# Kernel tuning notes

Hardware: AMD Instinct MI355X
Metric: run time of the kernel (lower is better)

## Reference

```python
import jax, jax.numpy as jnp
import numpy as np

DIM = 17  # LUT grid resolution per axis


def quad_interp(lut, x):
    """Quadrilinear (4D) LUT interpolation.
    lut: [C_out, D, D, D, D]; x: [B, 4, H, W] with values expected in [0, 1].
    Returns [B, C_out, H, W].
    """
    D = lut.shape[1]
    xs = jnp.clip(x, 0.0, 1.0) * (D - 1)          # [B,4,H,W]
    i0 = jnp.clip(jnp.floor(xs).astype(jnp.int32), 0, D - 2)
    f = xs - i0.astype(xs.dtype)                   # fractional part in [0,1]
    idx = [i0[:, k] for k in range(4)]             # each [B,H,W]
    frc = [f[:, k] for k in range(4)]
    out = None
    for corner in range(16):  # fixed 16-corner loop, not a data-dim loop
        ids, w = [], None
        for k in range(4):
            b = (corner >> k) & 1
            ids.append(idx[k] + b)
            wk = frc[k] if b else (1.0 - frc[k])
            w = wk if w is None else w * wk
        v = lut[:, ids[0], ids[1], ids[2], ids[3]]  # gather -> [C,B,H,W]
        term = v * w[None]
        out = term if out is None else out + term
    return jnp.transpose(out, (1, 0, 2, 3))        # [B,C,H,W]


def setup_inputs() -> dict:
    key = jax.random.key(0)
    ks = jax.random.split(key, 8)
    B, H, W = 8, 512, 512
    vi_image = jax.random.uniform(ks[0], (B, 3, H, W), dtype=jnp.float32)
    ir_image = jax.random.uniform(ks[1], (B, 1, H, W), dtype=jnp.float32)
    # Learned LUT tables (identity-style grids would live in [0,1]; use uniform)
    g = (DIM, DIM, DIM, DIM)
    lut8 = jax.random.uniform(ks[2], (4,) + g, dtype=jnp.float32)
    lut00 = jax.random.uniform(ks[3], (4,) + g, dtype=jnp.float32)
    lut01 = jax.random.uniform(ks[4], (4,) + g, dtype=jnp.float32)
    lut02 = jax.random.uniform(ks[5], (4,) + g, dtype=jnp.float32)
    lut03 = jax.random.uniform(ks[6], (4,) + g, dtype=jnp.float32)
    lutpgf = jax.random.uniform(ks[7], (3,) + g, dtype=jnp.float32)
    return {"vi_image": vi_image, "ir_image": ir_image, "lut8": lut8,
            "lut00": lut00, "lut01": lut01, "lut02": lut02,
            "lut03": lut03, "lutpgf": lutpgf}


def reference(vi_image, ir_image, lut8, lut00, lut01, lut02, lut03, lutpgf):
    x = jnp.concatenate([vi_image, ir_image], axis=1)   # [B,4,H,W]
    x = jnp.clip(quad_interp(lut8, x), 0.0, 1.0)        # hardtanh(0,1)
    x = jnp.clip(quad_interp(lut00, x), 0.0, 1.0)
    x = jnp.clip(quad_interp(lut01, x), 0.0, 1.0)
    x = jnp.clip(quad_interp(lut02, x), 0.0, 1.0)
    x = jnp.clip(quad_interp(lut03, x), 0.0, 1.0)
    return quad_interp(lutpgf, x)                       # [B,3,H,W]
```

## Files before the change

kernel.cpp:

```cpp
#include <hip/hip_runtime.h>

#pragma clang fp contract(off)

#define D4    83521
#define HW    262144
#define NPIX  2097152
#define QREC  73984
#define RECN  69632
#define CBLK  64

struct SrcPtrs { const float* p[6]; };

__global__ __launch_bounds__(256) void pack_oct_all(SrcPtrs sp,
                                                    float4* __restrict__ dst) {
    const int PER = RECN * 8;
    int j = blockIdx.x * 256 + threadIdx.x;
    int s = j / PER;
    int r = j - s * PER;
    int g = r & 7;
    int e = r >> 3;
    int i3 = e & 15;
    int i2 = (e >> 4) & 15;
    int i1 = (e >> 8) & 15;
    int i0 = e >> 12;
    int o = i0 * 4913 + i1 * 289 + i2 * 17 + i3
          + ((g >> 2) & 1) * 289 + ((g >> 1) & 1) * 17 + (g & 1);
    const float* __restrict__ src = sp.p[s];
    float4 v;
    v.x = src[o];
    v.y = src[D4 + o];
    v.z = src[2 * D4 + o];
    v.w = (s != 5) ? src[3 * D4 + o] : 0.f;
    dst[j] = v;
}

__global__ __launch_bounds__(CBLK) void fused_coop(const float* __restrict__ vi,
                                                   const float* __restrict__ ir,
                                                   const float4* __restrict__ luts,
                                                   float* __restrict__ out) {
#pragma clang fp contract(off)
    __shared__ float4 exch[CBLK * 17];

    int tid = threadIdx.x;
    int p = blockIdx.x * CBLK + tid;
    int b  = p >> 18;
    int hw = p & (HW - 1);
    int vbase = (b * 3) << 18;

    float x0 = vi[vbase + hw];
    float x1 = vi[vbase + HW + hw];
    float x2 = vi[vbase + 2 * HW + hw];
    float x3 = ir[p];

    int sub  = tid >> 4;
    int kidx = tid & 15;
    int b0   = (kidx >> 2) & 1;
    int slot = ((kidx >> 3) & 1) * 4 + (kidx & 1) * 2 + ((kidx >> 1) & 1);

    for (int s = 0; s < 6; ++s) {
        const float4* __restrict__ lutS =
            luts + (size_t)s * (RECN * 8) + b0 * (4096 * 8) + slot;

        x0 = fminf(fmaxf(x0, 0.f), 1.f);
        x1 = fminf(fmaxf(x1, 0.f), 1.f);
        x2 = fminf(fmaxf(x2, 0.f), 1.f);
        x3 = fminf(fmaxf(x3, 0.f), 1.f);
        float xs0 = x0 * 16.f;
        float xs1 = x1 * 16.f;
        float xs2 = x2 * 16.f;
        float xs3 = x3 * 16.f;
        int i0 = (int)xs0; i0 = i0 > 15 ? 15 : i0;
        int i1 = (int)xs1; i1 = i1 > 15 ? 15 : i1;
        int i2 = (int)xs2; i2 = i2 > 15 ? 15 : i2;
        int i3 = (int)xs3; i3 = i3 > 15 ? 15 : i3;
        float f0 = xs0 - (float)i0;
        float f1 = xs1 - (float)i1;
        float f2 = xs2 - (float)i2;
        float f3 = xs3 - (float)i3;
        float g0 = 1.f - f0;
        float g1 = 1.f - f1;
        float g2 = 1.f - f2;
        float g3 = 1.f - f3;
        float w01[4] = { g0 * g1, f0 * g1, g0 * f1, f0 * f1 };

        int r00 = ((i0 * 16 + i1) * 16 + i2) * 16 + i3;

        int r0s[16];
#pragma unroll
        for (int t = 0; t < 16; ++t)
            r0s[t] = __shfl(r00, 4 * t + sub, 64);

        float4 v[16];
#pragma unroll
        for (int t = 0; t < 16; ++t)
            v[t] = lutS[(size_t)r0s[t] * 8];
        __builtin_amdgcn_sched_barrier(0);

#pragma unroll
        for (int t = 0; t < 16; ++t)
            exch[(4 * t + sub) * 17 + kidx] = v[t];
        __builtin_amdgcn_sched_barrier(0);

        const float4* myb = &exch[tid * 17];
        float a0 = 0.f, a1 = 0.f, a2 = 0.f, a3 = 0.f;
#pragma unroll
        for (int hi = 0; hi < 2; ++hi) {
            float w3 = hi ? f3 : g3;
#pragma unroll
            for (int c = 0; c < 8; ++c) {
                int k = ((c & 3) << 2) + ((c >> 2) + 2 * hi);
                float4 vv = myb[k];
                float w012 = w01[c & 3] * ((c >> 2) ? f2 : g2);
                float w    = w012 * w3;
                if (hi == 0 && c == 0) {
                    a0 = vv.x * w; a1 = vv.y * w; a2 = vv.z * w; a3 = vv.w * w;
                } else {
                    a0 = a0 + vv.x * w; a1 = a1 + vv.y * w;
                    a2 = a2 + vv.z * w; a3 = a3 + vv.w * w;
                }
            }
        }
        __builtin_amdgcn_sched_barrier(0);
        x0 = a0; x1 = a1; x2 = a2; x3 = a3;
    }

    out[vbase + hw]          = x0;
    out[vbase + HW + hw]     = x1;
    out[vbase + 2 * HW + hw] = x2;
}

__global__ __launch_bounds__(256) void pack_quad(const float* __restrict__ src,
                                                 int n_ch,
                                                 float4* __restrict__ dst) {
    int e = blockIdx.x * 256 + threadIdx.x;
    if (e >= QREC) return;
    int i3 = e & 15;
    int i2 = (e >> 4) & 15;
    int t  = e >> 8;
    int i0 = t / 17;
    int i1 = t - i0 * 17;
    int base = i0 * 4913 + i1 * 289 + i2 * 17 + i3;
    float4* rec = dst + (size_t)e * 4;
#pragma unroll
    for (int g = 0; g < 4; ++g) {
        int o = base + (g & 1) * 17 + (g >> 1);
        float4 v;
        v.x = src[o];
        v.y = src[D4 + o];
        v.z = src[2 * D4 + o];
        v.w = (n_ch == 4) ? src[3 * D4 + o] : 0.f;
        rec[g] = v;
    }
}

__global__ __launch_bounds__(CBLK) void fused_coop_q(const float* __restrict__ vi,
                                                     const float* __restrict__ ir,
                                                     const float4* __restrict__ luts,
                                                     float* __restrict__ out) {
#pragma clang fp contract(off)
    __shared__ float4 exch[CBLK * 17];

    int tid = threadIdx.x;
    int p = blockIdx.x * CBLK + tid;
    int b  = p >> 18;
    int hw = p & (HW - 1);
    int vbase = (b * 3) << 18;

    float x0 = vi[vbase + hw];
    float x1 = vi[vbase + HW + hw];
    float x2 = vi[vbase + 2 * HW + hw];
    float x3 = ir[p];

    int rec     = (tid >> 2) & 3;
    int slot    = tid & 3;
    int rec_off = ((rec & 1) ? 4352 : 0) + ((rec & 2) ? 256 : 0);
    int sub     = tid >> 4;
    int kidx    = tid & 15;

    for (int s = 0; s < 6; ++s) {
        const float4* __restrict__ lutS =
            luts + (size_t)s * QREC * 4 + (size_t)rec_off * 4 + slot;

        x0 = fminf(fmaxf(x0, 0.f), 1.f);
        x1 = fminf(fmaxf(x1, 0.f), 1.f);
        x2 = fminf(fmaxf(x2, 0.f), 1.f);
        x3 = fminf(fmaxf(x3, 0.f), 1.f);
        float xs0 = x0 * 16.f;
        float xs1 = x1 * 16.f;
        float xs2 = x2 * 16.f;
        float xs3 = x3 * 16.f;
        int i0 = (int)xs0; i0 = i0 > 15 ? 15 : i0;
        int i1 = (int)xs1; i1 = i1 > 15 ? 15 : i1;
        int i2 = (int)xs2; i2 = i2 > 15 ? 15 : i2;
        int i3 = (int)xs3; i3 = i3 > 15 ? 15 : i3;
        float f0 = xs0 - (float)i0;
        float f1 = xs1 - (float)i1;
        float f2 = xs2 - (float)i2;
        float f3 = xs3 - (float)i3;
        float g0 = 1.f - f0;
        float g1 = 1.f - f1;
        float g2 = 1.f - f2;
        float g3 = 1.f - f3;
        float w01[4] = { g0 * g1, f0 * g1, g0 * f1, f0 * f1 };

        int r00 = ((i0 * 17 + i1) * 16 + i2) * 16 + i3;

        int r0s[16];
#pragma unroll
        for (int t = 0; t < 16; ++t)
            r0s[t] = __shfl(r00, 4 * t + sub, 64);

        float4 v[16];
#pragma unroll
        for (int t = 0; t < 16; ++t)
            v[t] = lutS[(size_t)r0s[t] * 4];
        __builtin_amdgcn_sched_barrier(0);

#pragma unroll
        for (int t = 0; t < 16; ++t)
            exch[(4 * t + sub) * 17 + kidx] = v[t];
        __builtin_amdgcn_sched_barrier(0);

        const float4* myb = &exch[tid * 17];
        float a0 = 0.f, a1 = 0.f, a2 = 0.f, a3 = 0.f;
#pragma unroll
        for (int hi = 0; hi < 2; ++hi) {
            float w3 = hi ? f3 : g3;
#pragma unroll
            for (int c = 0; c < 8; ++c) {
                int k = ((c & 3) << 2) + ((c >> 2) + 2 * hi);
                float4 vv = myb[k];
                float w012 = w01[c & 3] * ((c >> 2) ? f2 : g2);
                float w    = w012 * w3;
                if (hi == 0 && c == 0) {
                    a0 = vv.x * w; a1 = vv.y * w; a2 = vv.z * w; a3 = vv.w * w;
                } else {
                    a0 = a0 + vv.x * w; a1 = a1 + vv.y * w;
                    a2 = a2 + vv.z * w; a3 = a3 + vv.w * w;
                }
            }
        }
        __builtin_amdgcn_sched_barrier(0);
        x0 = a0; x1 = a1; x2 = a2; x3 = a3;
    }

    out[vbase + hw]          = x0;
    out[vbase + HW + hw]     = x1;
    out[vbase + 2 * HW + hw] = x2;
}

__global__ __launch_bounds__(256) void fused_fallback(const float* __restrict__ vi,
                                                      const float* __restrict__ ir,
                                                      const float* __restrict__ l8,
                                                      const float* __restrict__ l00,
                                                      const float* __restrict__ l01,
                                                      const float* __restrict__ l02,
                                                      const float* __restrict__ l03,
                                                      const float* __restrict__ lpgf,
                                                      float* __restrict__ out) {
#pragma clang fp contract(off)
    int p = blockIdx.x * 256 + threadIdx.x;
    if (p >= NPIX) return;
    int b  = p >> 18;
    int hw = p & (HW - 1);
    int vbase = (b * 3) << 18;

    const float* ptrs[6] = { l8, l00, l01, l02, l03, lpgf };

    float x0 = vi[vbase + hw];
    float x1 = vi[vbase + HW + hw];
    float x2 = vi[vbase + 2 * HW + hw];
    float x3 = ir[p];

    for (int s = 0; s < 6; ++s) {
        const float* __restrict__ L = ptrs[s];
        int n_ch = (s == 5) ? 3 : 4;
        x0 = fminf(fmaxf(x0, 0.f), 1.f);
        x1 = fminf(fmaxf(x1, 0.f), 1.f);
        x2 = fminf(fmaxf(x2, 0.f), 1.f);
        x3 = fminf(fmaxf(x3, 0.f), 1.f);
        float xs0 = x0 * 16.f;
        float xs1 = x1 * 16.f;
        float xs2 = x2 * 16.f;
        float xs3 = x3 * 16.f;
        int i0 = (int)xs0; i0 = i0 > 15 ? 15 : i0;
        int i1 = (int)xs1; i1 = i1 > 15 ? 15 : i1;
        int i2 = (int)xs2; i2 = i2 > 15 ? 15 : i2;
        int i3 = (int)xs3; i3 = i3 > 15 ? 15 : i3;
        float f0 = xs0 - (float)i0;
        float f1 = xs1 - (float)i1;
        float f2 = xs2 - (float)i2;
        float f3 = xs3 - (float)i3;
        float g0 = 1.f - f0;
        float g1 = 1.f - f1;
        float g2 = 1.f - f2;
        float g3 = 1.f - f3;
        float w01[4] = { g0 * g1, f0 * g1, g0 * f1, f0 * f1 };
        int off = i0 * 4913 + i1 * 289 + i2 * 17 + i3;
        float a0 = 0.f, a1 = 0.f, a2 = 0.f, a3 = 0.f;
        for (int cr = 0; cr < 16; ++cr) {
            int hi = cr >> 3, c = cr & 7;
            int idx = off + (c & 1) * 4913 + ((c >> 1) & 1) * 289 + (c >> 2) * 17 + hi;
            float w012 = w01[c & 3] * ((c >> 2) ? f2 : g2);
            float w    = w012 * (hi ? f3 : g3);
            float v0 = L[idx];
            float v1 = L[D4 + idx];
            float v2 = L[2 * D4 + idx];
            float v3 = (n_ch == 4) ? L[3 * D4 + idx] : 0.f;
            if (cr == 0) {
                a0 = v0 * w; a1 = v1 * w; a2 = v2 * w; a3 = v3 * w;
            } else {
                a0 = a0 + v0 * w; a1 = a1 + v1 * w;
                a2 = a2 + v2 * w; a3 = a3 + v3 * w;
            }
        }
        x0 = a0; x1 = a1; x2 = a2; x3 = a3;
    }

    out[vbase + hw]          = x0;
    out[vbase + HW + hw]     = x1;
    out[vbase + 2 * HW + hw] = x2;
}

extern "C" void kernel_launch(void* const* d_in, const int* in_sizes, int n_in,
                              void* d_out, int out_size, void* d_ws, size_t ws_size,
                              hipStream_t stream) {
    const float* vi = (const float*)d_in[0];
    const float* ir = (const float*)d_in[1];
    const float* raw[6] = {
        (const float*)d_in[2], (const float*)d_in[3],
        (const float*)d_in[4], (const float*)d_in[5],
        (const float*)d_in[6], (const float*)d_in[7]
    };
    float* out = (float*)d_out;

    const size_t OSZ      = (size_t)RECN * 128;
    const size_t NEED_OCT = 6 * OSZ;
    const size_t QSZ      = (size_t)QREC * 64;
    const size_t NEED_Q   = 6 * QSZ;

    if (ws_size >= NEED_OCT) {
        SrcPtrs sp;
        for (int s = 0; s < 6; ++s) sp.p[s] = raw[s];
        int pack_blocks = 6 * RECN * 8 / 256;
        pack_oct_all<<<pack_blocks, 256, 0, stream>>>(sp, (float4*)d_ws);
        fused_coop<<<NPIX / CBLK, CBLK, 0, stream>>>(vi, ir, (const float4*)d_ws, out);
    } else if (ws_size >= NEED_Q) {
        char* ws = (char*)d_ws;
        int pack_blocks = (QREC + 255) / 256;
        for (int s = 0; s < 6; ++s) {
            pack_quad<<<pack_blocks, 256, 0, stream>>>(raw[s], (s == 5) ? 3 : 4,
                                                       (float4*)(ws + s * QSZ));
        }
        fused_coop_q<<<NPIX / CBLK, CBLK, 0, stream>>>(vi, ir, (const float4*)ws, out);
    } else {
        fused_fallback<<<NPIX / 256, 256, 0, stream>>>(vi, ir, raw[0], raw[1], raw[2],
                                                       raw[3], raw[4], raw[5], out);
    }
}
```

Baseline: 278.8 us.

## Halve LDS exchange buffer by two-phase exchange and add occupancy hint

Splits the cooperative LDS exchange into two halves that reuse a 32-pixel buffer, so the shared-memory footprint per block is halved. Each half of the wavefront accumulates its interpolation in turn. The change also adds a min-blocks launch bound and replaces a per-thread integer division in the LUT pack kernel with a per-block one. More blocks should fit per CU, but half the lanes sit idle during each accumulation phase, which serializes the compute work.

```diff
diff --git a/kernel.cpp b/kernel.cpp
--- a/kernel.cpp
+++ b/kernel.cpp
@@ -14,8 +14,9 @@
 __global__ __launch_bounds__(256) void pack_oct_all(SrcPtrs sp,
                                                     float4* __restrict__ dst) {
     const int PER = RECN * 8;
-    int j = blockIdx.x * 256 + threadIdx.x;
-    int s = j / PER;
+    int blk = blockIdx.x;
+    int s = blk / 2176;
+    int j = blk * 256 + threadIdx.x;
     int r = j - s * PER;
     int g = r & 7;
     int e = r >> 3;
@@ -34,12 +35,12 @@
     dst[j] = v;
 }
 
-__global__ __launch_bounds__(CBLK) void fused_coop(const float* __restrict__ vi,
-                                                   const float* __restrict__ ir,
-                                                   const float4* __restrict__ luts,
-                                                   float* __restrict__ out) {
+__global__ __launch_bounds__(CBLK, 4) void fused_coop(const float* __restrict__ vi,
+                                                      const float* __restrict__ ir,
+                                                      const float4* __restrict__ luts,
+                                                      float* __restrict__ out) {
 #pragma clang fp contract(off)
-    __shared__ float4 exch[CBLK * 17];
+    __shared__ float4 exch[32 * 17];
 
     int tid = threadIdx.x;
     int p = blockIdx.x * CBLK + tid;
@@ -96,31 +97,62 @@
             v[t] = lutS[(size_t)r0s[t] * 8];
         __builtin_amdgcn_sched_barrier(0);
 
-#pragma unroll
-        for (int t = 0; t < 16; ++t)
+        float a0 = 0.f, a1 = 0.f, a2 = 0.f, a3 = 0.f;
+
+#pragma unroll
+        for (int t = 0; t < 8; ++t)
             exch[(4 * t + sub) * 17 + kidx] = v[t];
         __builtin_amdgcn_sched_barrier(0);
 
-        const float4* myb = &exch[tid * 17];
-        float a0 = 0.f, a1 = 0.f, a2 = 0.f, a3 = 0.f;
-#pragma unroll
-        for (int hi = 0; hi < 2; ++hi) {
-            float w3 = hi ? f3 : g3;
-#pragma unroll
-            for (int c = 0; c < 8; ++c) {
-                int k = ((c & 3) << 2) + ((c >> 2) + 2 * hi);
-                float4 vv = myb[k];
-                float w012 = w01[c & 3] * ((c >> 2) ? f2 : g2);
-                float w    = w012 * w3;
-                if (hi == 0 && c == 0) {
-                    a0 = vv.x * w; a1 = vv.y * w; a2 = vv.z * w; a3 = vv.w * w;
-                } else {
-                    a0 = a0 + vv.x * w; a1 = a1 + vv.y * w;
-                    a2 = a2 + vv.z * w; a3 = a3 + vv.w * w;
+        if (tid < 32) {
+            const float4* myb = &exch[tid * 17];
+#pragma unroll
+            for (int hi = 0; hi < 2; ++hi) {
+                float w3 = hi ? f3 : g3;
+#pragma unroll
+                for (int c = 0; c < 8; ++c) {
+                    int k = ((c & 3) << 2) + ((c >> 2) + 2 * hi);
+                    float4 vv = myb[k];
+                    float w012 = w01[c & 3] * ((c >> 2) ? f2 : g2);
+                    float w    = w012 * w3;
+                    if (hi == 0 && c == 0) {
+                        a0 = vv.x * w; a1 = vv.y * w; a2 = vv.z * w; a3 = vv.w * w;
+                    } else {
+                        a0 = a0 + vv.x * w; a1 = a1 + vv.y * w;
+                        a2 = a2 + vv.z * w; a3 = a3 + vv.w * w;
+                    }
                 }
             }
         }
         __builtin_amdgcn_sched_barrier(0);
+
+#pragma unroll
+        for (int t = 8; t < 16; ++t)
+            exch[(4 * (t - 8) + sub) * 17 + kidx] = v[t];
+        __builtin_amdgcn_sched_barrier(0);
+
+        if (tid >= 32) {
+            const float4* myb = &exch[(tid - 32) * 17];
+#pragma unroll
+            for (int hi = 0; hi < 2; ++hi) {
+                float w3 = hi ? f3 : g3;
+#pragma unroll
+                for (int c = 0; c < 8; ++c) {
+                    int k = ((c & 3) << 2) + ((c >> 2) + 2 * hi);
+                    float4 vv = myb[k];
+                    float w012 = w01[c & 3] * ((c >> 2) ? f2 : g2);
+                    float w    = w012 * w3;
+                    if (hi == 0 && c == 0) {
+                        a0 = vv.x * w; a1 = vv.y * w; a2 = vv.z * w; a3 = vv.w * w;
+                    } else {
+                        a0 = a0 + vv.x * w; a1 = a1 + vv.y * w;
+                        a2 = a2 + vv.z * w; a3 = a3 + vv.w * w;
+                    }
+                }
+            }
+        }
+        __builtin_amdgcn_sched_barrier(0);
+
         x0 = a0; x1 = a1; x2 = a2; x3 = a3;
     }
 
```

After: 323.1 us. +15.9%, slower.

## Load LUT corners directly into LDS with global_load_lds and XOR swizzle

Applied to the files above, without the earlier changes.

Replaces the register gather followed by the LDS store with direct global-to-LDS loads (global_load_lds, 16 bytes). This removes the VGPR round trip and the ds_write instructions. The padded 17-stride exchange layout becomes a 16-stride layout with an XOR swizzle on the corner index to avoid bank conflicts, and the per-lane offsets are precomputed once. The pack kernel also computes the stage index per block instead of per thread. Risks: depends on 16-byte LDS-direct load support, there is a full vmcnt wait, and there is no explicit barrier, which relies on single-wave blocks.

```diff
diff --git a/kernel.cpp b/kernel.cpp
--- a/kernel.cpp
+++ b/kernel.cpp
@@ -11,11 +11,15 @@
 
 struct SrcPtrs { const float* p[6]; };
 
+typedef const __attribute__((address_space(1))) void* gptr_t;
+typedef __attribute__((address_space(3))) void* lptr_t;
+
 __global__ __launch_bounds__(256) void pack_oct_all(SrcPtrs sp,
                                                     float4* __restrict__ dst) {
     const int PER = RECN * 8;
-    int j = blockIdx.x * 256 + threadIdx.x;
-    int s = j / PER;
+    int blk = blockIdx.x;
+    int s = blk / 2176;
+    int j = blk * 256 + threadIdx.x;
     int r = j - s * PER;
     int g = r & 7;
     int e = r >> 3;
@@ -39,7 +43,7 @@
                                                    const float4* __restrict__ luts,
                                                    float* __restrict__ out) {
 #pragma clang fp contract(off)
-    __shared__ float4 exch[CBLK * 17];
+    __shared__ float4 exch[CBLK * 16];
 
     int tid = threadIdx.x;
     int p = blockIdx.x * CBLK + tid;
@@ -52,14 +56,19 @@
     float x2 = vi[vbase + 2 * HW + hw];
     float x3 = ir[p];
 
-    int sub  = tid >> 4;
-    int kidx = tid & 15;
-    int b0   = (kidx >> 2) & 1;
-    int slot = ((kidx >> 3) & 1) * 4 + (kidx & 1) * 2 + ((kidx >> 1) & 1);
+    int sub = tid >> 4;
+    int lo  = tid & 15;
+
+    int aoff[16];
+#pragma unroll
+    for (int t = 0; t < 16; ++t) {
+        int c = lo ^ ((4 * t + sub) & 15);
+        aoff[t] = ((c >> 2) & 1) * (4096 * 8)
+                + ((c >> 3) & 1) * 4 + (c & 1) * 2 + ((c >> 1) & 1);
+    }
 
     for (int s = 0; s < 6; ++s) {
-        const float4* __restrict__ lutS =
-            luts + (size_t)s * (RECN * 8) + b0 * (4096 * 8) + slot;
+        const float4* __restrict__ lutS4 = luts + (size_t)s * (RECN * 8);
 
         x0 = fminf(fmaxf(x0, 0.f), 1.f);
         x1 = fminf(fmaxf(x1, 0.f), 1.f);
@@ -90,18 +99,18 @@
         for (int t = 0; t < 16; ++t)
             r0s[t] = __shfl(r00, 4 * t + sub, 64);
 
-        float4 v[16];
-#pragma unroll
-        for (int t = 0; t < 16; ++t)
-            v[t] = lutS[(size_t)r0s[t] * 8];
-        __builtin_amdgcn_sched_barrier(0);
-
-#pragma unroll
-        for (int t = 0; t < 16; ++t)
-            exch[(4 * t + sub) * 17 + kidx] = v[t];
-        __builtin_amdgcn_sched_barrier(0);
-
-        const float4* myb = &exch[tid * 17];
+#pragma unroll
+        for (int t = 0; t < 16; ++t) {
+            const float4* gp = lutS4 + ((size_t)r0s[t] * 8 + aoff[t]);
+            __builtin_amdgcn_global_load_lds((gptr_t)gp,
+                                             (lptr_t)&exch[t * 64],
+                                             16, 0, 0);
+        }
+        __builtin_amdgcn_sched_barrier(0);
+        asm volatile("s_waitcnt vmcnt(0)" ::: "memory");
+        __builtin_amdgcn_sched_barrier(0);
+
+        const float4* myb = &exch[tid * 16];
         float a0 = 0.f, a1 = 0.f, a2 = 0.f, a3 = 0.f;
 #pragma unroll
         for (int hi = 0; hi < 2; ++hi) {
@@ -109,7 +118,7 @@
 #pragma unroll
             for (int c = 0; c < 8; ++c) {
                 int k = ((c & 3) << 2) + ((c >> 2) + 2 * hi);
-                float4 vv = myb[k];
+                float4 vv = myb[k ^ lo];
                 float w012 = w01[c & 3] * ((c >> 2) ? f2 : g2);
                 float w    = w012 * w3;
                 if (hi == 0 && c == 0) {
```

Result: no change. 276.3 us (-0.9%).
